# Kernel optimization log

Measured on AMD Instinct MI355X. Metric: run time of the kernel, lower is better.

The kernel has to match this reference:

```python
import jax, jax.numpy as jnp
import numpy as np

N = 4096      # num_nodes
DIN = 16      # num_inputs
C = 16        # comm_channels
CHQ = 8       # ch_q
K = 10        # value-iteration steps
GAMMA = 0.99
EPS = float(np.finfo(np.float32).eps)


def setup_inputs() -> dict:
    key = jax.random.key(0)
    ks = jax.random.split(key, 8)
    x = jax.random.normal(ks[0], (N, DIN), dtype=jnp.float32)
    comms = jnp.zeros((N, C), dtype=jnp.float32)  # fresh comm state (reset())
    # random symmetric 0/1 adjacency, ~20 avg degree, zero diagonal
    u = jax.random.uniform(ks[1], (N, N), dtype=jnp.float32)
    a = (u < 0.005).astype(jnp.float32)
    adj = jnp.maximum(a, a.T) * (1.0 - jnp.eye(N, dtype=jnp.float32))
    mask = jnp.ones((N,), dtype=jnp.float32)
    # parameters (torch Linear: y = x @ W + b, weights stored [in, out] here)
    Wr = jax.random.normal(ks[2], (DIN + C, 1), dtype=jnp.float32) * 0.1   # reward_encoding
    br = jnp.zeros((1,), dtype=jnp.float32)
    We = jax.random.normal(ks[3], (DIN + C, CHQ), dtype=jnp.float32) * 0.1  # encoder
    be = jnp.zeros((CHQ,), dtype=jnp.float32)
    w_emb = jax.random.normal(ks[4], (CHQ,), dtype=jnp.float32) * 0.1       # embedder (ch_q -> 1)
    b_emb = jnp.zeros((), dtype=jnp.float32)
    Wa = jax.random.normal(ks[5], (CHQ,), dtype=jnp.float32) * 0.1          # action_decoding (1 -> ch_q)
    ba = jnp.zeros((CHQ,), dtype=jnp.float32)
    return dict(x=x, comms=comms, adj=adj, mask=mask, Wr=Wr, br=br,
                We=We, be=be, w_emb=w_emb, b_emb=b_emb, Wa=Wa, ba=ba, k=K)


def reference(x, comms, adj, mask, Wr, br, We, be, w_emb, b_emb, Wa, ba, k):
    n = adj.shape[0]
    # initialize_adj: symmetric normalization D^{-1/2} (A + I) D^{-1/2}
    a_norm = adj + jnp.eye(n, dtype=adj.dtype)
    deg = a_norm.sum(axis=0)
    dinv_sqrt = jnp.sqrt(1.0 / (deg + EPS))
    k3 = a_norm * dinv_sqrt[:, None] * dinv_sqrt[None, :]

    xc = jnp.concatenate([x, comms], axis=1)          # [n, DIN+C]
    r = (xc @ Wr + br)[:, 0]                          # reward per node [n]
    # embedder(cols - rows) fused: score[i,j] = s[j] - s[i] + b_emb
    s = (xc @ We + be) @ w_emb                        # [n]
    kernel3 = k3 * (s[None, :] - s[:, None] + b_emb)  # [n, n]

    # k-step value iteration
    v = jnp.zeros_like(r)
    for _ in range(k):
        k3v = kernel3 @ (r + GAMMA * v)               # [n]
        q = k3v[:, None] * Wa[None, :] + ba           # action_decoding (1 -> ch_q): [n, ch_q]
        v = q.max(axis=-1)                            # [n]

    # final_feature_process (rl=False): additive -inf mask
    return v + jnp.where(mask == 0, -jnp.inf, 0.0)
```

## Files before the change

### kernel.cpp

```cpp
#include <hip/hip_runtime.h>
#include <math.h>

#define NN     4096
#define NB     256
#define TPB    1024
#define WPB    16
#define CAP    128
#define GAMMA  0.99f
#define EPSF   1.1920929e-07f
#define KSTEPS 10
#define REP    4
#define LSTR   8


__device__ __forceinline__ unsigned long long pk2(float lo, float hi) {
    return ((unsigned long long)__float_as_uint(hi) << 32) |
            (unsigned long long)__float_as_uint(lo);
}
__device__ __forceinline__ float lo_f(unsigned long long z) {
    return __uint_as_float((unsigned int)z);
}
__device__ __forceinline__ float hi_f(unsigned long long z) {
    return __uint_as_float((unsigned int)(z >> 32));
}
__device__ __forceinline__ unsigned long long pkVT(float v, int tag) {
    return ((unsigned long long)(unsigned int)tag << 32) |
            (unsigned long long)__float_as_uint(v);
}
__device__ __forceinline__ int tag_of(unsigned long long z) {
    return (int)(unsigned int)(z >> 32);
}

__global__ void __launch_bounds__(TPB) gvin_flow(
    const float* __restrict__ adj,  const float* __restrict__ x,
    const float* __restrict__ comms,const float* __restrict__ mask,
    const float* __restrict__ Wr,   const float* __restrict__ br,
    const float* __restrict__ We,   const float* __restrict__ be,
    const float* __restrict__ w_emb,const float* __restrict__ b_emb,
    const float* __restrict__ Wa,   const float* __restrict__ ba,
    unsigned long long* PD, unsigned long long* U0, unsigned long long* U1,
    float* __restrict__ out)
{
    __shared__ int nbr[WPB][CAP];
    __shared__ int lcnt[WPB];
    const int wave = threadIdx.x >> 6;
    const int lane = threadIdx.x & 63;
    const int g = (int)blockIdx.x * WPB + wave;

    if (lane == 0) { lcnt[wave] = 1; nbr[wave][0] = g; }

    const float4* rowp = (const float4*)(adj + (size_t)g * NN);
#pragma unroll 4
    for (int it = 0; it < 16; ++it) {
        const float4 v = rowp[lane + it * 64];
        const int b4 = (lane + it * 64) * 4;
        if (v.x != 0.0f) { int sl = atomicAdd(&lcnt[wave], 1); if (sl < CAP) nbr[wave][sl] = b4;     }
        if (v.y != 0.0f) { int sl = atomicAdd(&lcnt[wave], 1); if (sl < CAP) nbr[wave][sl] = b4 + 1; }
        if (v.z != 0.0f) { int sl = atomicAdd(&lcnt[wave], 1); if (sl < CAP) nbr[wave][sl] = b4 + 2; }
        if (v.w != 0.0f) { int sl = atomicAdd(&lcnt[wave], 1); if (sl < CAP) nbr[wave][sl] = b4 + 3; }
    }

    float pr = 0.0f, ps = 0.0f;
    if (lane < 32) {
        const float xc = (lane < 16) ? x[g * 16 + lane] : comms[g * 16 + (lane - 16)];
        float we = 0.0f;
#pragma unroll
        for (int c = 0; c < 8; ++c) we += We[lane * 8 + c] * w_emb[c];
        pr = xc * Wr[lane];
        ps = xc * we;
    } else if (lane == 32) {
#pragma unroll
        for (int c = 0; c < 8; ++c) ps += be[c] * w_emb[c];
        pr = br[0];
    }
#pragma unroll
    for (int off = 32; off; off >>= 1) { pr += __shfl_xor(pr, off); ps += __shfl_xor(ps, off); }
    const float r = pr, s = ps;

    const int   deg  = lcnt[wave];
    const int   cl   = deg < CAP ? deg : CAP;
    const float dinv = sqrtf(1.0f / ((float)deg + EPSF));
    const float p    = dinv * (s + b_emb[0]);

    if (lane < REP) {
        const size_t line = ((size_t)g * REP + lane) * LSTR;
        __hip_atomic_store(PD + line, pk2(p, dinv),
                           __ATOMIC_RELAXED, __HIP_MEMORY_SCOPE_AGENT);
        __hip_atomic_store(U0 + line, pkVT(r, 0),
                           __ATOMIC_RELAXED, __HIP_MEMORY_SCOPE_AGENT);
    }

    const bool val0 = lane < cl;
    const bool val1 = 64 + lane < cl;
    const int  j0   = val0 ? nbr[wave][lane] : g;
    const int  j1   = val1 ? nbr[wave][64 + lane] : g;
    const int  rep  = g & (REP - 1);
    const size_t e0 = ((size_t)j0 * REP + rep) * LSTR;
    const size_t e1 = ((size_t)j1 * REP + rep) * LSTR;

    float wa[8], bb[8];
#pragma unroll
    for (int c = 0; c < 8; ++c) { wa[c] = Wa[c]; bb[c] = ba[c]; }

    float p0 = 0.0f, d0 = 0.0f, p1 = 0.0f, d1 = 0.0f;
    {
        bool n0 = val0, n1 = val1;
        while (__any(n0 | n1)) {
            if (n0) {
                const unsigned long long z = __hip_atomic_load(
                    PD + e0, __ATOMIC_RELAXED, __HIP_MEMORY_SCOPE_AGENT);
                const float dv = hi_f(z);
                if (dv > 0.0f) { p0 = lo_f(z); d0 = dv; n0 = false; }
            }
            if (n1) {
                const unsigned long long z = __hip_atomic_load(
                    PD + e1, __ATOMIC_RELAXED, __HIP_MEMORY_SCOPE_AGENT);
                const float dv = hi_f(z);
                if (dv > 0.0f) { p1 = lo_f(z); d1 = dv; n1 = false; }
            }
            if (__any(n0 | n1)) __builtin_amdgcn_s_sleep(1);
        }
    }

    float v = 0.0f;
    for (int t = 0; t < KSTEPS; ++t) {
        unsigned long long* Uin  = (t & 1) ? U1 : U0;
        unsigned long long* Uout = (t & 1) ? U0 : U1;
        float a1 = 0.0f, a2 = 0.0f;
        bool n0 = val0, n1 = val1;
        while (__any(n0 | n1)) {
            if (n0) {
                const unsigned long long z = __hip_atomic_load(
                    Uin + e0, __ATOMIC_RELAXED, __HIP_MEMORY_SCOPE_AGENT);
                if (tag_of(z) == t) {
                    const float u = lo_f(z);
                    a1 = fmaf(p0, u, a1); a2 = fmaf(d0, u, a2); n0 = false;
                }
            }
            if (n1) {
                const unsigned long long z = __hip_atomic_load(
                    Uin + e1, __ATOMIC_RELAXED, __HIP_MEMORY_SCOPE_AGENT);
                if (tag_of(z) == t) {
                    const float u = lo_f(z);
                    a1 = fmaf(p1, u, a1); a2 = fmaf(d1, u, a2); n1 = false;
                }
            }
            if (__any(n0 | n1)) __builtin_amdgcn_s_sleep(1);
        }
#pragma unroll
        for (int off = 32; off; off >>= 1) { a1 += __shfl_xor(a1, off); a2 += __shfl_xor(a2, off); }
        const float k3v = dinv * (a1 - s * a2);
        v = fmaf(k3v, wa[0], bb[0]);
#pragma unroll
        for (int c = 1; c < 8; ++c) v = fmaxf(v, fmaf(k3v, wa[c], bb[c]));
        if (t < KSTEPS - 1 && lane < REP) {
            const float u = r + GAMMA * v;
            __hip_atomic_store(Uout + ((size_t)g * REP + lane) * LSTR, pkVT(u, t + 1),
                               __ATOMIC_RELAXED, __HIP_MEMORY_SCOPE_AGENT);
        }
    }

    if (lane == 0) out[g] = v + (mask[g] == 0.0f ? -INFINITY : 0.0f);
}

extern "C" void kernel_launch(void* const* d_in, const int* in_sizes, int n_in,
                              void* d_out, int out_size, void* d_ws, size_t ws_size,
                              hipStream_t stream) {
    const float* x     = (const float*)d_in[0];
    const float* comms = (const float*)d_in[1];
    const float* adj   = (const float*)d_in[2];
    const float* mask  = (const float*)d_in[3];
    const float* Wr    = (const float*)d_in[4];
    const float* br    = (const float*)d_in[5];
    const float* We    = (const float*)d_in[6];
    const float* be    = (const float*)d_in[7];
    const float* w_emb = (const float*)d_in[8];
    const float* b_emb = (const float*)d_in[9];
    const float* Wa    = (const float*)d_in[10];
    const float* ba    = (const float*)d_in[11];

    char* ws = (char*)d_ws;
    const size_t PLANE = (size_t)NN * REP * 64;
    unsigned long long* PD = (unsigned long long*)(ws);
    unsigned long long* U0 = (unsigned long long*)(ws + PLANE);
    unsigned long long* U1 = (unsigned long long*)(ws + 2 * PLANE);
    float* out = (float*)d_out;

    gvin_flow<<<dim3(NB), dim3(TPB), 0, stream>>>(
        adj, x, comms, mask, Wr, br, We, be, w_emb, b_emb, Wa, ba,
        PD, U0, U1, out);
}
```

Measured before the change: 171.7 us.

## Sweep dense value vector into LDS per step instead of per-neighbor polling

The per-step value vector is now stored densely (one 8-byte tagged entry per node) rather than replicated across cache-line-strided slots. Each block does a coalesced bulk copy of the whole input vector into shared memory each iteration, so most neighbor gathers hit LDS. Only entries whose tag is stale are re-polled from global memory. This adds two block barriers per step plus a 32KB LDS buffer, and dense packing puts many writers on shared cache lines, which may raise contention.

```diff
diff --git a/kernel.cpp b/kernel.cpp
--- a/kernel.cpp
+++ b/kernel.cpp
@@ -9,9 +9,10 @@
 #define GAMMA  0.99f
 #define EPSF   1.1920929e-07f
 #define KSTEPS 10
-#define REP    4
-#define LSTR   8
+#define PDSTR  8
 
+
+union F2U { unsigned long long u; float2 f; };
 
 __device__ __forceinline__ unsigned long long pk2(float lo, float hi) {
     return ((unsigned long long)__float_as_uint(hi) << 32) |
@@ -31,7 +32,7 @@
     return (int)(unsigned int)(z >> 32);
 }
 
-__global__ void __launch_bounds__(TPB) gvin_flow(
+__global__ void __launch_bounds__(TPB) gvin_sweep(
     const float* __restrict__ adj,  const float* __restrict__ x,
     const float* __restrict__ comms,const float* __restrict__ mask,
     const float* __restrict__ Wr,   const float* __restrict__ br,
@@ -43,6 +44,7 @@
 {
     __shared__ int nbr[WPB][CAP];
     __shared__ int lcnt[WPB];
+    __shared__ unsigned long long ULDS[NN];
     const int wave = threadIdx.x >> 6;
     const int lane = threadIdx.x & 63;
     const int g = (int)blockIdx.x * WPB + wave;
@@ -82,11 +84,10 @@
     const float dinv = sqrtf(1.0f / ((float)deg + EPSF));
     const float p    = dinv * (s + b_emb[0]);
 
-    if (lane < REP) {
-        const size_t line = ((size_t)g * REP + lane) * LSTR;
-        __hip_atomic_store(PD + line, pk2(p, dinv),
+    if (lane == 0) {
+        __hip_atomic_store(PD + (size_t)g * PDSTR, pk2(p, dinv),
                            __ATOMIC_RELAXED, __HIP_MEMORY_SCOPE_AGENT);
-        __hip_atomic_store(U0 + line, pkVT(r, 0),
+        __hip_atomic_store(U0 + g, pkVT(r, 0),
                            __ATOMIC_RELAXED, __HIP_MEMORY_SCOPE_AGENT);
     }
 
@@ -94,9 +95,6 @@
     const bool val1 = 64 + lane < cl;
     const int  j0   = val0 ? nbr[wave][lane] : g;
     const int  j1   = val1 ? nbr[wave][64 + lane] : g;
-    const int  rep  = g & (REP - 1);
-    const size_t e0 = ((size_t)j0 * REP + rep) * LSTR;
-    const size_t e1 = ((size_t)j1 * REP + rep) * LSTR;
 
     float wa[8], bb[8];
 #pragma unroll
@@ -108,13 +106,13 @@
         while (__any(n0 | n1)) {
             if (n0) {
                 const unsigned long long z = __hip_atomic_load(
-                    PD + e0, __ATOMIC_RELAXED, __HIP_MEMORY_SCOPE_AGENT);
+                    PD + (size_t)j0 * PDSTR, __ATOMIC_RELAXED, __HIP_MEMORY_SCOPE_AGENT);
                 const float dv = hi_f(z);
                 if (dv > 0.0f) { p0 = lo_f(z); d0 = dv; n0 = false; }
             }
             if (n1) {
                 const unsigned long long z = __hip_atomic_load(
-                    PD + e1, __ATOMIC_RELAXED, __HIP_MEMORY_SCOPE_AGENT);
+                    PD + (size_t)j1 * PDSTR, __ATOMIC_RELAXED, __HIP_MEMORY_SCOPE_AGENT);
                 const float dv = hi_f(z);
                 if (dv > 0.0f) { p1 = lo_f(z); d1 = dv; n1 = false; }
             }
@@ -126,36 +124,43 @@
     for (int t = 0; t < KSTEPS; ++t) {
         unsigned long long* Uin  = (t & 1) ? U1 : U0;
         unsigned long long* Uout = (t & 1) ? U0 : U1;
-        float a1 = 0.0f, a2 = 0.0f;
-        bool n0 = val0, n1 = val1;
+
+        __syncthreads();
+#pragma unroll
+        for (int w = 0; w < NN / TPB; ++w) {
+            const int idx = (int)threadIdx.x + (w << 10);
+            ULDS[idx] = __hip_atomic_load(Uin + idx, __ATOMIC_RELAXED,
+                                          __HIP_MEMORY_SCOPE_AGENT);
+        }
+        __syncthreads();
+
+        unsigned long long z0 = ULDS[j0];
+        unsigned long long z1 = ULDS[j1];
+        bool n0 = val0 && (tag_of(z0) != t);
+        bool n1 = val1 && (tag_of(z1) != t);
         while (__any(n0 | n1)) {
             if (n0) {
-                const unsigned long long z = __hip_atomic_load(
-                    Uin + e0, __ATOMIC_RELAXED, __HIP_MEMORY_SCOPE_AGENT);
-                if (tag_of(z) == t) {
-                    const float u = lo_f(z);
-                    a1 = fmaf(p0, u, a1); a2 = fmaf(d0, u, a2); n0 = false;
-                }
+                z0 = __hip_atomic_load(Uin + j0, __ATOMIC_RELAXED, __HIP_MEMORY_SCOPE_AGENT);
+                n0 = (tag_of(z0) != t);
             }
             if (n1) {
-                const unsigned long long z = __hip_atomic_load(
-                    Uin + e1, __ATOMIC_RELAXED, __HIP_MEMORY_SCOPE_AGENT);
-                if (tag_of(z) == t) {
-                    const float u = lo_f(z);
-                    a1 = fmaf(p1, u, a1); a2 = fmaf(d1, u, a2); n1 = false;
-                }
+                z1 = __hip_atomic_load(Uin + j1, __ATOMIC_RELAXED, __HIP_MEMORY_SCOPE_AGENT);
+                n1 = (tag_of(z1) != t);
             }
             if (__any(n0 | n1)) __builtin_amdgcn_s_sleep(1);
         }
+
+        const float u0f = val0 ? lo_f(z0) : 0.0f;
+        float a1 = p0 * u0f, a2 = d0 * u0f;
+        if (val1) { const float u1f = lo_f(z1); a1 = fmaf(p1, u1f, a1); a2 = fmaf(d1, u1f, a2); }
 #pragma unroll
         for (int off = 32; off; off >>= 1) { a1 += __shfl_xor(a1, off); a2 += __shfl_xor(a2, off); }
         const float k3v = dinv * (a1 - s * a2);
         v = fmaf(k3v, wa[0], bb[0]);
 #pragma unroll
         for (int c = 1; c < 8; ++c) v = fmaxf(v, fmaf(k3v, wa[c], bb[c]));
-        if (t < KSTEPS - 1 && lane < REP) {
-            const float u = r + GAMMA * v;
-            __hip_atomic_store(Uout + ((size_t)g * REP + lane) * LSTR, pkVT(u, t + 1),
+        if (t < KSTEPS - 1 && lane == 0) {
+            __hip_atomic_store(Uout + g, pkVT(r + GAMMA * v, t + 1),
                                __ATOMIC_RELAXED, __HIP_MEMORY_SCOPE_AGENT);
         }
     }
@@ -180,13 +185,12 @@
     const float* ba    = (const float*)d_in[11];
 
     char* ws = (char*)d_ws;
-    const size_t PLANE = (size_t)NN * REP * 64;
     unsigned long long* PD = (unsigned long long*)(ws);
-    unsigned long long* U0 = (unsigned long long*)(ws + PLANE);
-    unsigned long long* U1 = (unsigned long long*)(ws + 2 * PLANE);
+    unsigned long long* U0 = (unsigned long long*)(ws + (size_t)NN * 64);
+    unsigned long long* U1 = (unsigned long long*)(ws + (size_t)NN * 64 + (size_t)NN * 8);
     float* out = (float*)d_out;
 
-    gvin_flow<<<dim3(NB), dim3(TPB), 0, stream>>>(
+    gvin_sweep<<<dim3(NB), dim3(TPB), 0, stream>>>(
         adj, x, comms, mask, Wr, br, We, be, w_emb, b_emb, Wa, ba,
         PD, U0, U1, out);
 }
```

Result: faster. 161.1 us (-6.2%).
